# Optimization experiments

Measured on AMD Instinct MI355X. Metric: run time of the kernel, lower is better.

## Reference

```python
import jax, jax.numpy as jnp
import numpy as np

B, S, D = 4, 4096, 1024          # batch, seq, in/out features
H = 128                          # controller_hidden_dim
K = 8                            # num_spectral_bases
R = 8                            # low_rank_rank
OR = 8                           # orthogonal_rank
RES_SCALE = 1.0; SPEC_SCALE = 1.0; LR_SCALE = 1.0; ROT_SCALE = 1.0
LN_EPS = 1e-5


def setup_inputs() -> dict:
    key = jax.random.key(0)
    ks = jax.random.split(key, 16)
    g = lambda k, shape, scale=0.02: jax.random.normal(k, shape, jnp.float32) * scale
    return dict(
        x=jax.random.normal(ks[0], (B, S, D), jnp.float32),
        # base linear (teacher-aligned base)
        W_base=g(ks[1], (D, D)), b_base=jnp.zeros((D,), jnp.float32),
        # pooled-token conditioner: LayerNorm -> Linear -> GELU -> Linear
        ln_g=jnp.ones((D,), jnp.float32), ln_b=jnp.zeros((D,), jnp.float32),
        Wc1=g(ks[2], (D, H)), bc1=jnp.zeros((H,), jnp.float32),
        Wc2=g(ks[3], (H, H)), bc2=jnp.zeros((H,), jnp.float32),
        # gate heads
        W_rot_gate=g(ks[4], (H, 1)), b_rot_gate=jnp.zeros((1,), jnp.float32),
        W_rot_coeff=g(ks[5], (H, OR)), b_rot_coeff=jnp.zeros((OR,), jnp.float32),
        W_spec_gate=g(ks[6], (H, K)), b_spec_gate=jnp.zeros((K,), jnp.float32),
        W_lr_coeff=g(ks[7], (H, R)), b_lr_coeff=jnp.zeros((R,), jnp.float32),
        # spectral basis operator: input basis U, output basis V
        U_spec=g(ks[8], (K, D), 0.05), V_spec=g(ks[9], (K, D), 0.05),
        # low-rank residual operator
        U_lr=g(ks[10], (R, D), 0.05), V_lr=g(ks[11], (R, D), 0.05),
        # low-rank orthogonal mixer generators (skew-symmetric pairs)
        A_orth=g(ks[12], (OR, D), 0.05), B_orth=g(ks[13], (OR, D), 0.05),
    )


def reference(x, W_base, b_base, ln_g, ln_b, Wc1, bc1, Wc2, bc2,
              W_rot_gate, b_rot_gate, W_rot_coeff, b_rot_coeff,
              W_spec_gate, b_spec_gate, W_lr_coeff, b_lr_coeff,
              U_spec, V_spec, U_lr, V_lr, A_orth, B_orth):
    # --- pooled token conditioner: mean pool -> LN -> MLP -> hidden h [B,H]
    pooled = x.mean(axis=1)                                   # [B, D]
    mu = pooled.mean(-1, keepdims=True)
    var = pooled.var(-1, keepdims=True)
    z = (pooled - mu) * jax.lax.rsqrt(var + LN_EPS) * ln_g + ln_b
    h = jax.nn.gelu(z @ Wc1 + bc1) @ Wc2 + bc2                # [B, H]

    # --- conditioner-produced gates
    rot_gate = jax.nn.sigmoid(h @ W_rot_gate + b_rot_gate)    # [B, 1]
    rot_coeff = jnp.tanh(h @ W_rot_coeff + b_rot_coeff)       # [B, OR]
    spec_gate = jnp.tanh(h @ W_spec_gate + b_spec_gate)       # [B, K]
    lr_coeff = jnp.tanh(h @ W_lr_coeff + b_lr_coeff)          # [B, R]

    # --- low-rank orthogonal mixer: x_rot = x + gate * x @ G^T,
    #     G = sum_k c_k (a_k b_k^T - b_k a_k^T) (skew-symmetric generator)
    pa = jnp.einsum('bsi,ki->bsk', x, A_orth)
    pb = jnp.einsum('bsi,ki->bsk', x, B_orth)
    rot = (jnp.einsum('bsk,bk,ki->bsi', pb, rot_coeff, A_orth)
           - jnp.einsum('bsk,bk,ki->bsi', pa, rot_coeff, B_orth))
    x_rot = x + (ROT_SCALE * rot_gate)[:, None, :] * rot      # [B,S,D]

    # --- spectral basis operator: gated rank-K map through fixed bases
    s = jnp.einsum('bsi,ki->bsk', x_rot, U_spec)
    y_spec = SPEC_SCALE * jnp.einsum('bsk,bk,ko->bso', s, spec_gate, V_spec)

    # --- low-rank residual operator
    t = jnp.einsum('bsi,ki->bsk', x_rot, U_lr)
    y_lr = LR_SCALE * jnp.einsum('bsk,bk,ko->bso', t, lr_coeff, V_lr)

    # --- teacher-aligned base + gated residual operators
    return x_rot @ W_base + b_base + RES_SCALE * (y_spec + y_lr)
```

## Files before the change

kernel.cpp:

```cpp
#include <hip/hip_runtime.h>

typedef unsigned short u16;
typedef unsigned int   u32;
typedef __bf16 bf16x8 __attribute__((ext_vector_type(8)));
typedef float  f32x4  __attribute__((ext_vector_type(4)));

#define DD 1024

__device__ __forceinline__ u16 f2bf(float f) {
  u32 u = __float_as_uint(f);
  u32 r = (u + 0x7FFFu + ((u >> 16) & 1u)) >> 16;
  return (u16)r;
}

typedef const __attribute__((address_space(1))) void* gp1;
typedef __attribute__((address_space(3))) void* lp3;
__device__ __forceinline__ void gll16(const void* g, void* l) {
  __builtin_amdgcn_global_load_lds((gp1)g, (lp3)l, 16, 0, 0);
}

template <bool XB>
__global__ __launch_bounds__(256) void k01_pre(
    const float* __restrict__ x, u16* __restrict__ xb, float* __restrict__ pooled,
    const float* __restrict__ W,
    const float* __restrict__ Ao, const float* __restrict__ Bo,
    const float* __restrict__ Us, const float* __restrict__ Ul,
    float* __restrict__ AWBW, float* __restrict__ Mbuf,
    u16* __restrict__ Pb, u16* __restrict__ Wt) {
  const int tid = threadIdx.x;
  const int bid = blockIdx.x;
  if (bid >= 296) {
    const int i = bid - 296;
    const int xcd = i & 7, local = i >> 3;
    const int rb = xcd * 128 + local;
    const int b = rb >> 8;
    const long r0 = (long)rb * 16;
    const int c0 = tid * 4;
    float s0 = 0.f, s1 = 0.f, s2 = 0.f, s3 = 0.f;
    for (int r = 0; r < 16; r++) {
      float4 v = *(const float4*)(x + (r0 + r) * DD + c0);
      if (XB) {
        ushort4 o;
        o.x = f2bf(v.x); o.y = f2bf(v.y); o.z = f2bf(v.z); o.w = f2bf(v.w);
        *(ushort4*)(xb + (r0 + r) * DD + c0) = o;
      }
      s0 += v.x; s1 += v.y; s2 += v.z; s3 += v.w;
    }
    atomicAdd(&pooled[b * DD + c0 + 0], s0);
    atomicAdd(&pooled[b * DD + c0 + 1], s1);
    atomicAdd(&pooled[b * DD + c0 + 2], s2);
    atomicAdd(&pooled[b * DD + c0 + 3], s3);
    return;
  }
  if (bid < 32) {
    __shared__ float red2[2][128][16];
    const int m = bid;
    const int n = (m & 7) * 128 + (tid & 127), q = m >> 3, ih = tid >> 7;
    float acc[16];
#pragma unroll
    for (int k = 0; k < 16; k++) acc[k] = 0.f;
    const int ib = q * 256 + ih * 128;
    for (int i = ib; i < ib + 128; i++) {
      float wv = W[(long)i * DD + n];
#pragma unroll
      for (int k = 0; k < 8; k++) {
        acc[k]     += Ao[k * DD + i] * wv;
        acc[k + 8] += Bo[k * DD + i] * wv;
      }
    }
#pragma unroll
    for (int k = 0; k < 16; k++) red2[ih][tid & 127][k] = acc[k];
    __syncthreads();
    if (ih == 0)
#pragma unroll
      for (int k = 0; k < 16; k++)
        atomicAdd(&AWBW[k * DD + n], red2[0][tid][k] + red2[1][tid][k]);
  } else if (bid < 36) {
    __shared__ float red[64][4];
    const int m = bid - 32;
    const float* L  = (m == 0 || m == 2) ? Ao : Bo;
    const float* Rr = (m < 2) ? Us : Ul;
    const int o = tid >> 2, ch = tid & 3;
    const int k = o >> 3, kp = o & 7;
    float a = 0.f;
    for (int i = ch * 256; i < ch * 256 + 256; i++)
      a += L[(long)k * DD + i] * Rr[(long)kp * DD + i];
    red[o][ch] = a;
    __syncthreads();
    if (tid < 64) Mbuf[m * 64 + tid] = red[tid][0] + red[tid][1] + red[tid][2] + red[tid][3];
  } else if (bid < 40) {
    const int m = bid - 36;
    const float* src = m == 0 ? Ao : m == 1 ? Bo : m == 2 ? Us : Ul;
#pragma unroll
    for (int j = 0; j < 8; j++)
      for (int q = 0; q < 4; q++) {
        int i = q * 256 + tid;
        Pb[(m * 8 + j) * DD + i] = f2bf(src[j * DD + i]);
      }
  } else {
    __shared__ u16 T[64][66];
    const int t = bid - 40, tr = t >> 4, tc = t & 15;
#pragma unroll
    for (int q2 = 0; q2 < 16; q2++) {
      int idx = q2 * 256 + tid, r = idx >> 6, c = idx & 63;
      T[r][c] = f2bf(W[(long)(tr * 64 + r) * DD + tc * 64 + c]);
    }
    __syncthreads();
#pragma unroll
    for (int q2 = 0; q2 < 16; q2++) {
      int idx = q2 * 256 + tid, c = idx >> 6, r = idx & 63;
      Wt[(long)(tc * 64 + c) * DD + tr * 64 + r] = T[r][c];
    }
  }
}

__global__ __launch_bounds__(256) void k2ab(
    const float* __restrict__ pooledsum,
    const float* __restrict__ lng, const float* __restrict__ lnb,
    const float* __restrict__ Wc1, float* __restrict__ h1pre,
    const float* __restrict__ AWBW, const float* Vs, const float* Vl,
    const float* bc1, const float* Wc2, const float* bc2,
    const float* Wrg, const float* brg, const float* Wrc, const float* brc,
    const float* Wsg, const float* bsg, const float* Wlc, const float* blc,
    float* __restrict__ gates, u16* __restrict__ RwT,
    u32* __restrict__ cnt) {
  const int tid = threadIdx.x;
  if (blockIdx.x < 32) {
    __shared__ float zs[1024];
    __shared__ float red[256];
    const int b = blockIdx.x >> 3, ch = blockIdx.x & 7;
    float4 v = *(const float4*)(pooledsum + b * DD + tid * 4);
    v.x *= (1.f / 4096.f); v.y *= (1.f / 4096.f); v.z *= (1.f / 4096.f); v.w *= (1.f / 4096.f);
    float s = v.x + v.y + v.z + v.w;
    float sq = v.x * v.x + v.y * v.y + v.z * v.z + v.w * v.w;
    red[tid] = s; __syncthreads();
    for (int st = 128; st > 0; st >>= 1) { if (tid < st) red[tid] += red[tid + st]; __syncthreads(); }
    float mu = red[0] * (1.f / 1024.f);
    __syncthreads();
    red[tid] = sq; __syncthreads();
    for (int st = 128; st > 0; st >>= 1) { if (tid < st) red[tid] += red[tid + st]; __syncthreads(); }
    float var = red[0] * (1.f / 1024.f) - mu * mu;
    float rs = rsqrtf(var + 1e-5f);
    __syncthreads();
    {
      float4 g = *(const float4*)(lng + tid * 4);
      float4 be = *(const float4*)(lnb + tid * 4);
      zs[tid * 4 + 0] = (v.x - mu) * rs * g.x + be.x;
      zs[tid * 4 + 1] = (v.y - mu) * rs * g.y + be.y;
      zs[tid * 4 + 2] = (v.z - mu) * rs * g.z + be.z;
      zs[tid * 4 + 3] = (v.w - mu) * rs * g.w + be.w;
    }
    __syncthreads();
    const int j = tid & 127, half = tid >> 7;
    float a = 0.f;
#pragma unroll 8
    for (int dd = 0; dd < 64; dd++) {
      int ldi = half * 64 + dd;
      a += zs[ch * 128 + ldi] * Wc1[(long)ch * 16384 + ldi * 128 + j];
    }
    red[tid] = a;
    __syncthreads();
    if (tid < 128) atomicAdd(&h1pre[b * 128 + tid], red[tid] + red[tid + 128]);
    __syncthreads();
    if (tid == 0) atomicAdd(cnt, 1u);
  } else if (blockIdx.x < 36) {
    __shared__ float h1s[128], hb[128];
    __shared__ float red[256];
    const int b = (int)blockIdx.x - 32;
    if (tid == 0) {
      while (atomicAdd(cnt, 0u) < 32u) __builtin_amdgcn_s_sleep(8);
    }
    __syncthreads();
    if (tid < 128) {
      float hv = atomicAdd(&h1pre[b * 128 + tid], 0.f) + bc1[tid];
      float th = tanhf(0.7978845608028654f * (hv + 0.044715f * hv * hv * hv));
      h1s[tid] = 0.5f * hv * (1.f + th);
    }
    __syncthreads();
    const int i = tid & 127, half = tid >> 7;
    float a = 0.f;
#pragma unroll 8
    for (int k = 0; k < 64; k++) {
      int kk = half * 64 + k;
      a += h1s[kk] * Wc2[kk * 128 + i];
    }
    red[tid] = a;
    __syncthreads();
    if (tid < 128) hb[tid] = red[tid] + red[tid + 128] + bc2[tid];
    __syncthreads();
    if (tid < 25) {
      float acc;
      if (tid == 0) {
        acc = brg[0];
        for (int k = 0; k < 128; k++) acc += hb[k] * Wrg[k];
        red[0] = 1.f / (1.f + expf(-acc));
      } else if (tid < 9) {
        int ci = tid - 1; acc = brc[ci];
        for (int k = 0; k < 128; k++) acc += hb[k] * Wrc[k * 8 + ci];
        red[tid] = tanhf(acc);
      } else if (tid < 17) {
        int ci = tid - 9; acc = bsg[ci];
        for (int k = 0; k < 128; k++) acc += hb[k] * Wsg[k * 8 + ci];
        red[tid] = tanhf(acc);
      } else {
        int ci = tid - 17; acc = blc[ci];
        for (int k = 0; k < 128; k++) acc += hb[k] * Wlc[k * 8 + ci];
        red[tid] = tanhf(acc);
      }
    }
    __syncthreads();
    if (tid < 24) {
      float g = red[0];
      gates[b * 32 + tid] = (tid < 8) ? g * red[1 + tid] : red[1 + tid];
    }
  } else {
    const int n = (int)(blockIdx.x - 36) * 256 + tid;
#pragma unroll
    for (int j = 0; j < 8; j++) {
      RwT[n * 32 + j]      = f2bf(AWBW[j * DD + n]);
      RwT[n * 32 + 8 + j]  = f2bf(AWBW[(8 + j) * DD + n]);
      RwT[n * 32 + 16 + j] = f2bf(Vs[(long)j * DD + n]);
      RwT[n * 32 + 24 + j] = f2bf(Vl[(long)j * DD + n]);
    }
  }
}

__global__ __launch_bounds__(256, 2) void k3b_fused(
    const u16* __restrict__ xb, const u16* __restrict__ Wt,
    const u16* __restrict__ Pb, const float* __restrict__ gates,
    const float* __restrict__ Mbuf, const u16* __restrict__ RwT,
    const float* __restrict__ bb, float* __restrict__ out) {
  __shared__ __align__(16) char smem[54400];
  const int tid = threadIdx.x, lane = tid & 63, w = tid >> 6;
  const int quad = lane >> 4, lrow = lane & 15;
  const int g = blockIdx.x;
  const int xcd = g & 7, local = g >> 3;
  const int bm = xcd * 16 + (local >> 2);
  const int bn2 = local & 3;
  const long m0 = (long)bm * 128;
  const int n0 = bn2 * 256;
  const int batch = bm >> 5;
  float* Ml = (float*)(smem + 53248);
  float* gl = (float*)(smem + 54272);
  Ml[tid] = Mbuf[tid];
  if (tid < 24) gl[tid] = gates[batch * 32 + tid];
  const int mw = (w & 1) * 64, nw = (w >> 1) * 128;
  const int pc0 = (w >> 1) * 16;
  const int sr = lane >> 2, sc = (lane & 3) * 16;
  const char* xbp = (const char*)xb;
  const char* wtp = (const char*)Wt;
  const char* pbp = (const char*)Pb;
  const long aOff0 = (m0 + (long)w * 16 + sr) * 2048 + sc;
  const long aOff1 = aOff0 + 64 * 2048;
  const long bOff  = ((long)n0 + w * 16 + sr) * 2048 + sc;
  const long pOff  = ((long)w * 16 + sr) * 2048 + sc;
  const int d0 = w * 1024 + lane * 16;

  f32x4 acc[4][8] = {};
  f32x4 acc2[4] = {};

  gll16(xbp + aOff0, smem + d0);
  gll16(xbp + aOff1, smem + d0 + 4096);
#pragma unroll
  for (int seg = 0; seg < 4; seg++)
    gll16(wtp + bOff + (long)seg * 64 * 2048, smem + 16384 + seg * 4096 + d0);
  if (w < 2) gll16(pbp + pOff, smem + 49152 + d0);
  __syncthreads();

  int cur = 0;
  for (int kc = 0; kc < 32; kc++) {
    if (kc < 31) {
      const long ko = (long)(kc + 1) * 64;
      const int s = cur ^ 1;
      gll16(xbp + aOff0 + ko, smem + s * 8192 + d0);
      gll16(xbp + aOff1 + ko, smem + s * 8192 + d0 + 4096);
#pragma unroll
      for (int seg = 0; seg < 4; seg++)
        gll16(wtp + bOff + (long)seg * 64 * 2048 + ko,
              smem + 16384 + s * 16384 + seg * 4096 + d0);
      if (w < 2) gll16(pbp + pOff + ko, smem + 49152 + s * 2048 + d0);
    }
    const u16* At = (const u16*)(smem + cur * 8192);
    const u16* Bt = (const u16*)(smem + 16384 + cur * 16384);
    const u16* Pt = (const u16*)(smem + 49152 + cur * 2048);
    bf16x8 af[4], bq[8], bp;
#pragma unroll
    for (int tm = 0; tm < 4; tm++)
      af[tm] = *(const bf16x8*)(At + (mw + tm * 16 + lrow) * 32 + quad * 8);
#pragma unroll
    for (int tn = 0; tn < 8; tn++)
      bq[tn] = *(const bf16x8*)(Bt + (nw + tn * 16 + lrow) * 32 + quad * 8);
    bp = *(const bf16x8*)(Pt + (pc0 + lrow) * 32 + quad * 8);
#pragma unroll
    for (int tm = 0; tm < 4; tm++)
#pragma unroll
      for (int tn = 0; tn < 8; tn++)
        acc[tm][tn] = __builtin_amdgcn_mfma_f32_16x16x32_bf16(af[tm], bq[tn], acc[tm][tn], 0, 0, 0);
#pragma unroll
    for (int tm = 0; tm < 4; tm++)
      acc2[tm] = __builtin_amdgcn_mfma_f32_16x16x32_bf16(af[tm], bp, acc2[tm], 0, 0, 0);
    __syncthreads();
    cur ^= 1;
  }

  {
    const long rOff = ((long)n0 + w * 16 + sr) * 64 + sc;
#pragma unroll
    for (int seg = 0; seg < 4; seg++)
      gll16((const char*)RwT + rOff + (long)seg * 64 * 64,
            smem + 16384 + seg * 4096 + d0);
  }
  float* projF = (float*)smem;
#pragma unroll
  for (int tm = 0; tm < 4; tm++)
#pragma unroll
    for (int r = 0; r < 4; r++) {
      int row = mw + tm * 16 + quad * 4 + r;
      int col = pc0 + lrow;
      projF[row * 32 + (col ^ (row & 31))] = acc2[tm][r];
    }
  __syncthreads();
  if (tid < 128) {
    float pr[32];
#pragma unroll
    for (int j = 0; j < 32; j++) pr[j] = projF[tid * 32 + (j ^ (tid & 31))];
    float wo[32];
#pragma unroll
    for (int k = 0; k < 8; k++) { wo[k] = gl[k] * pr[8 + k]; wo[8 + k] = -gl[k] * pr[k]; }
#pragma unroll
    for (int kp = 0; kp < 8; kp++) {
      float sv = pr[16 + kp], tv = pr[24 + kp];
#pragma unroll
      for (int k = 0; k < 8; k++) {
        float gpb = gl[k] * pr[8 + k], gpa = gl[k] * pr[k];
        sv += gpb * Ml[k * 8 + kp]       - gpa * Ml[64 + k * 8 + kp];
        tv += gpb * Ml[128 + k * 8 + kp] - gpa * Ml[192 + k * 8 + kp];
      }
      wo[16 + kp] = gl[8 + kp] * sv;
      wo[24 + kp] = gl[16 + kp] * tv;
    }
    u16* wLds = (u16*)(smem + 32768);
#pragma unroll
    for (int j = 0; j < 32; j++) wLds[tid * 32 + j] = f2bf(wo[j]);
  }
  __syncthreads();
  {
    const u16* wL = (const u16*)(smem + 32768);
    const u16* Rt = (const u16*)(smem + 16384);
    bf16x8 af[4], bq[8];
#pragma unroll
    for (int tm = 0; tm < 4; tm++)
      af[tm] = *(const bf16x8*)(wL + (mw + tm * 16 + lrow) * 32 + quad * 8);
#pragma unroll
    for (int tn = 0; tn < 8; tn++)
      bq[tn] = *(const bf16x8*)(Rt + (nw + tn * 16 + lrow) * 32 + quad * 8);
#pragma unroll
    for (int tm = 0; tm < 4; tm++)
#pragma unroll
      for (int tn = 0; tn < 8; tn++)
        acc[tm][tn] = __builtin_amdgcn_mfma_f32_16x16x32_bf16(af[tm], bq[tn], acc[tm][tn], 0, 0, 0);
  }
#pragma unroll
  for (int tn = 0; tn < 8; tn++) {
    const int col = n0 + nw + tn * 16 + lrow;
    const float bias = bb[col];
#pragma unroll
    for (int tm = 0; tm < 4; tm++)
#pragma unroll
      for (int r = 0; r < 4; r++) {
        long row = m0 + mw + tm * 16 + quad * 4 + r;
        out[row * DD + col] = acc[tm][tn][r] + bias;
      }
  }
}

template <bool XB>
__global__ __launch_bounds__(256) void k3_fused(
    const float* __restrict__ xf, const u16* __restrict__ xb,
    const u16* __restrict__ Wt, const u16* __restrict__ Pb,
    const float* __restrict__ gates, const float* __restrict__ Mbuf,
    const u16* __restrict__ RwT, const float* __restrict__ bb,
    float* __restrict__ out) {
  __shared__ __align__(16) u16 At[4096];
  __shared__ __align__(16) u16 Bt[4096];
  __shared__ __align__(16) u16 Pt[1024];
  __shared__ float projF[128 * 32];
  __shared__ __align__(16) u16 wLds[4096];
  __shared__ float Ml[256];
  __shared__ float gl[24];
  const int tid = threadIdx.x, lane = tid & 63, w = tid >> 6;
  const int quad = lane >> 4, lrow = lane & 15;
  const int bn = blockIdx.x & 7, bm = blockIdx.x >> 3;
  const long m0 = (long)bm * 128;
  const int n0 = bn * 128;
  const int batch = bm >> 5;
  Ml[tid] = Mbuf[tid];
  if (tid < 24) gl[tid] = gates[batch * 32 + tid];
  const int mw = (w & 1) * 64, nw = (w >> 1) * 64;
  const int p0 = (w * 2) * 1024 + lane * 16, p1 = p0 + 1024;
  f32x4 acc[4][4] = {};
  f32x4 acc2[2][2] = {};
  for (int kc = 0; kc < 32; kc++) {
    uint4 vb0 = *(const uint4*)((const char*)Wt + (long)(n0 + (p0 >> 6)) * 2048 + kc * 64 + (p0 & 63));
    uint4 vb1 = *(const uint4*)((const char*)Wt + (long)(n0 + (p1 >> 6)) * 2048 + kc * 64 + (p1 & 63));
    uint4 vp;
    if (tid < 128)
      vp = *(const uint4*)((const char*)Pb + (tid >> 2) * 2048 + kc * 64 + (tid & 3) * 16);
    if (XB) {
      uint4 va0 = *(const uint4*)((const char*)xb + (m0 + (p0 >> 6)) * 2048 + kc * 64 + (p0 & 63));
      uint4 va1 = *(const uint4*)((const char*)xb + (m0 + (p1 >> 6)) * 2048 + kc * 64 + (p1 & 63));
      *(uint4*)((char*)At + p0) = va0;
      *(uint4*)((char*)At + p1) = va1;
    } else {
      ushort4 oa[4];
#pragma unroll
      for (int i = 0; i < 4; i++) {
        int fi = i * 256 + tid, row = fi >> 3, c4 = (fi & 7) * 4;
        float4 v = *(const float4*)(xf + (m0 + row) * DD + kc * 32 + c4);
        oa[i].x = f2bf(v.x); oa[i].y = f2bf(v.y); oa[i].z = f2bf(v.z); oa[i].w = f2bf(v.w);
      }
#pragma unroll
      for (int i = 0; i < 4; i++) {
        int fi = i * 256 + tid, row = fi >> 3, c4 = (fi & 7) * 4;
        *(ushort4*)(At + row * 32 + c4) = oa[i];
      }
    }
    *(uint4*)((char*)Bt + p0) = vb0;
    *(uint4*)((char*)Bt + p1) = vb1;
    if (tid < 128) *(uint4*)((char*)Pt + (tid >> 2) * 64 + (tid & 3) * 16) = vp;
    __syncthreads();
    bf16x8 af[4], bq[4], af2[2], bp[2];
#pragma unroll
    for (int tm = 0; tm < 4; tm++)
      af[tm] = *(const bf16x8*)(At + (mw + tm * 16 + lrow) * 32 + quad * 8);
#pragma unroll
    for (int tn = 0; tn < 4; tn++)
      bq[tn] = *(const bf16x8*)(Bt + (nw + tn * 16 + lrow) * 32 + quad * 8);
#pragma unroll
    for (int t2 = 0; t2 < 2; t2++)
      af2[t2] = *(const bf16x8*)(At + (w * 32 + t2 * 16 + lrow) * 32 + quad * 8);
#pragma unroll
    for (int tn2 = 0; tn2 < 2; tn2++)
      bp[tn2] = *(const bf16x8*)(Pt + (tn2 * 16 + lrow) * 32 + quad * 8);
#pragma unroll
    for (int tm = 0; tm < 4; tm++)
#pragma unroll
      for (int tn = 0; tn < 4; tn++)
        acc[tm][tn] = __builtin_amdgcn_mfma_f32_16x16x32_bf16(af[tm], bq[tn], acc[tm][tn], 0, 0, 0);
#pragma unroll
    for (int t2 = 0; t2 < 2; t2++)
#pragma unroll
      for (int tn2 = 0; tn2 < 2; tn2++)
        acc2[t2][tn2] = __builtin_amdgcn_mfma_f32_16x16x32_bf16(af2[t2], bp[tn2], acc2[t2][tn2], 0, 0, 0);
    __syncthreads();
  }
#pragma unroll
  for (int t2 = 0; t2 < 2; t2++)
#pragma unroll
    for (int tn2 = 0; tn2 < 2; tn2++)
#pragma unroll
      for (int r = 0; r < 4; r++)
        projF[(w * 32 + t2 * 16 + quad * 4 + r) * 32 + tn2 * 16 + lrow] = acc2[t2][tn2][r];
  {
    uint4 vr0 = *(const uint4*)((const char*)RwT + (long)(n0 + (p0 >> 6)) * 64 + (p0 & 63));
    uint4 vr1 = *(const uint4*)((const char*)RwT + (long)(n0 + (p1 >> 6)) * 64 + (p1 & 63));
    *(uint4*)((char*)Bt + p0) = vr0;
    *(uint4*)((char*)Bt + p1) = vr1;
  }
  __syncthreads();
  if (tid < 128) {
    float pr[32];
#pragma unroll
    for (int j = 0; j < 32; j++) pr[j] = projF[tid * 32 + j];
    float wo[32];
#pragma unroll
    for (int k = 0; k < 8; k++) { wo[k] = gl[k] * pr[8 + k]; wo[8 + k] = -gl[k] * pr[k]; }
#pragma unroll
    for (int kp = 0; kp < 8; kp++) {
      float sv = pr[16 + kp], tv = pr[24 + kp];
#pragma unroll
      for (int k = 0; k < 8; k++) {
        float gpb = gl[k] * pr[8 + k], gpa = gl[k] * pr[k];
        sv += gpb * Ml[k * 8 + kp]       - gpa * Ml[64 + k * 8 + kp];
        tv += gpb * Ml[128 + k * 8 + kp] - gpa * Ml[192 + k * 8 + kp];
      }
      wo[16 + kp] = gl[8 + kp] * sv;
      wo[24 + kp] = gl[16 + kp] * tv;
    }
#pragma unroll
    for (int j = 0; j < 32; j++) wLds[tid * 32 + j] = f2bf(wo[j]);
  }
  __syncthreads();
  {
    bf16x8 af[4], bq[4];
#pragma unroll
    for (int tm = 0; tm < 4; tm++)
      af[tm] = *(const bf16x8*)(wLds + (mw + tm * 16 + lrow) * 32 + quad * 8);
#pragma unroll
    for (int tn = 0; tn < 4; tn++)
      bq[tn] = *(const bf16x8*)(Bt + (nw + tn * 16 + lrow) * 32 + quad * 8);
#pragma unroll
    for (int tm = 0; tm < 4; tm++)
#pragma unroll
      for (int tn = 0; tn < 4; tn++)
        acc[tm][tn] = __builtin_amdgcn_mfma_f32_16x16x32_bf16(af[tm], bq[tn], acc[tm][tn], 0, 0, 0);
  }
#pragma unroll
  for (int tn = 0; tn < 4; tn++) {
    const int col = n0 + nw + tn * 16 + lrow;
    const float bias = bb[col];
#pragma unroll
    for (int tm = 0; tm < 4; tm++)
#pragma unroll
      for (int r = 0; r < 4; r++) {
        long row = m0 + mw + tm * 16 + quad * 4 + r;
        out[row * DD + col] = acc[tm][tn][r] + bias;
      }
  }
}

extern "C" void kernel_launch(void* const* d_in, const int* in_sizes, int n_in,
                              void* d_out, int out_size, void* d_ws, size_t ws_size,
                              hipStream_t stream) {
  const float* x   = (const float*)d_in[0];
  const float* Wb  = (const float*)d_in[1];
  const float* bb  = (const float*)d_in[2];
  const float* lng = (const float*)d_in[3];
  const float* lnb = (const float*)d_in[4];
  const float* Wc1 = (const float*)d_in[5];
  const float* bc1 = (const float*)d_in[6];
  const float* Wc2 = (const float*)d_in[7];
  const float* bc2 = (const float*)d_in[8];
  const float* Wrg = (const float*)d_in[9];
  const float* brg = (const float*)d_in[10];
  const float* Wrc = (const float*)d_in[11];
  const float* brc = (const float*)d_in[12];
  const float* Wsg = (const float*)d_in[13];
  const float* bsg = (const float*)d_in[14];
  const float* Wlc = (const float*)d_in[15];
  const float* blc = (const float*)d_in[16];
  const float* Us  = (const float*)d_in[17];
  const float* Vs  = (const float*)d_in[18];
  const float* Ul  = (const float*)d_in[19];
  const float* Vl  = (const float*)d_in[20];
  const float* Ao  = (const float*)d_in[21];
  const float* Bo  = (const float*)d_in[22];

  char* ws = (char*)d_ws;
  float* pooled = (float*)(ws + 0);
  float* AWBW   = (float*)(ws + 16384);
  float* h1pre  = (float*)(ws + 81920);
  float* gates  = (float*)(ws + 83968);
  float* Mbuf   = (float*)(ws + 84480);
  u32*   cntH   = (u32*)  (ws + 85504);
  u16*   RwT    = (u16*)  (ws + 85568);
  u16*   Pb     = (u16*)  (ws + 151104);
  u16*   Wt     = (u16*)  (ws + 216640);
  u16*   xb     = (u16*)  (ws + 2313792);
  float* out    = (float*)d_out;

  const bool modeA = ws_size >= (size_t)2313792 + 33554432;

  (void)hipMemsetAsync(d_ws, 0, 85568, stream);
  if (modeA) {
    k01_pre<true><<<1320, 256, 0, stream>>>(x, xb, pooled, Wb, Ao, Bo, Us, Ul,
                                            AWBW, Mbuf, Pb, Wt);
    k2ab<<<40, 256, 0, stream>>>(pooled, lng, lnb, Wc1, h1pre,
                                 AWBW, Vs, Vl, bc1, Wc2, bc2,
                                 Wrg, brg, Wrc, brc, Wsg, bsg, Wlc, blc,
                                 gates, RwT, cntH);
    k3b_fused<<<512, 256, 0, stream>>>(xb, Wt, Pb, gates, Mbuf, RwT, bb, out);
  } else {
    k01_pre<false><<<1320, 256, 0, stream>>>(x, xb, pooled, Wb, Ao, Bo, Us, Ul,
                                             AWBW, Mbuf, Pb, Wt);
    k2ab<<<40, 256, 0, stream>>>(pooled, lng, lnb, Wc1, h1pre,
                                 AWBW, Vs, Vl, bc1, Wc2, bc2,
                                 Wrg, brg, Wrc, brc, Wsg, bsg, Wlc, blc,
                                 gates, RwT, cntH);
    k3_fused<false><<<1024, 256, 0, stream>>>(x, xb, Wt, Pb, gates, Mbuf, RwT, bb, out);
  }
}
```

Before: 311.4 us.

## Split preprocessing into weight-prep and x-streaming kernels, widen AW/BW projection grid

The fused preprocessing kernel is split into two launches: one for weight-derived work (AW/BW projection, small Gram products, bf16 packing, W transpose) and one that streams x to bf16 and accumulates the pooled sums. The AW/BW projection now uses 64 blocks, each covering half as many input rows, which shortens the long-running blocks that previously held up the combined grid. Static shared arrays are merged into one aliased buffer so fewer LDS bytes are reserved per block. The cost is an extra kernel launch and the loss of overlap between the two kinds of work within a single grid.

```diff
diff --git a/kernel.cpp b/kernel.cpp
--- a/kernel.cpp
+++ b/kernel.cpp
@@ -19,48 +19,24 @@
   __builtin_amdgcn_global_load_lds((gp1)g, (lp3)l, 16, 0, 0);
 }
 
-template <bool XB>
-__global__ __launch_bounds__(256) void k01_pre(
-    const float* __restrict__ x, u16* __restrict__ xb, float* __restrict__ pooled,
+__global__ __launch_bounds__(256) void kA_heavy(
     const float* __restrict__ W,
     const float* __restrict__ Ao, const float* __restrict__ Bo,
     const float* __restrict__ Us, const float* __restrict__ Ul,
     float* __restrict__ AWBW, float* __restrict__ Mbuf,
     u16* __restrict__ Pb, u16* __restrict__ Wt) {
+  __shared__ __align__(16) char shb[16384];
   const int tid = threadIdx.x;
   const int bid = blockIdx.x;
-  if (bid >= 296) {
-    const int i = bid - 296;
-    const int xcd = i & 7, local = i >> 3;
-    const int rb = xcd * 128 + local;
-    const int b = rb >> 8;
-    const long r0 = (long)rb * 16;
-    const int c0 = tid * 4;
-    float s0 = 0.f, s1 = 0.f, s2 = 0.f, s3 = 0.f;
-    for (int r = 0; r < 16; r++) {
-      float4 v = *(const float4*)(x + (r0 + r) * DD + c0);
-      if (XB) {
-        ushort4 o;
-        o.x = f2bf(v.x); o.y = f2bf(v.y); o.z = f2bf(v.z); o.w = f2bf(v.w);
-        *(ushort4*)(xb + (r0 + r) * DD + c0) = o;
-      }
-      s0 += v.x; s1 += v.y; s2 += v.z; s3 += v.w;
-    }
-    atomicAdd(&pooled[b * DD + c0 + 0], s0);
-    atomicAdd(&pooled[b * DD + c0 + 1], s1);
-    atomicAdd(&pooled[b * DD + c0 + 2], s2);
-    atomicAdd(&pooled[b * DD + c0 + 3], s3);
-    return;
-  }
-  if (bid < 32) {
-    __shared__ float red2[2][128][16];
+  if (bid < 64) {
+    float (*red2)[128][16] = (float (*)[128][16])shb;
     const int m = bid;
     const int n = (m & 7) * 128 + (tid & 127), q = m >> 3, ih = tid >> 7;
     float acc[16];
 #pragma unroll
     for (int k = 0; k < 16; k++) acc[k] = 0.f;
-    const int ib = q * 256 + ih * 128;
-    for (int i = ib; i < ib + 128; i++) {
+    const int ib = q * 128 + ih * 64;
+    for (int i = ib; i < ib + 64; i++) {
       float wv = W[(long)i * DD + n];
 #pragma unroll
       for (int k = 0; k < 8; k++) {
@@ -75,9 +51,9 @@
 #pragma unroll
       for (int k = 0; k < 16; k++)
         atomicAdd(&AWBW[k * DD + n], red2[0][tid][k] + red2[1][tid][k]);
-  } else if (bid < 36) {
-    __shared__ float red[64][4];
-    const int m = bid - 32;
+  } else if (bid < 68) {
+    float (*red)[4] = (float (*)[4])shb;
+    const int m = bid - 64;
     const float* L  = (m == 0 || m == 2) ? Ao : Bo;
     const float* Rr = (m < 2) ? Us : Ul;
     const int o = tid >> 2, ch = tid & 3;
@@ -88,8 +64,8 @@
     red[o][ch] = a;
     __syncthreads();
     if (tid < 64) Mbuf[m * 64 + tid] = red[tid][0] + red[tid][1] + red[tid][2] + red[tid][3];
-  } else if (bid < 40) {
-    const int m = bid - 36;
+  } else if (bid < 72) {
+    const int m = bid - 68;
     const float* src = m == 0 ? Ao : m == 1 ? Bo : m == 2 ? Us : Ul;
 #pragma unroll
     for (int j = 0; j < 8; j++)
@@ -98,8 +74,8 @@
         Pb[(m * 8 + j) * DD + i] = f2bf(src[j * DD + i]);
       }
   } else {
-    __shared__ u16 T[64][66];
-    const int t = bid - 40, tr = t >> 4, tc = t & 15;
+    u16 (*T)[66] = (u16 (*)[66])shb;
+    const int t = bid - 72, tr = t >> 4, tc = t & 15;
 #pragma unroll
     for (int q2 = 0; q2 < 16; q2++) {
       int idx = q2 * 256 + tid, r = idx >> 6, c = idx & 63;
@@ -112,6 +88,32 @@
       Wt[(long)(tc * 64 + c) * DD + tr * 64 + r] = T[r][c];
     }
   }
+}
+
+template <bool XB>
+__global__ __launch_bounds__(256) void kB_stream(
+    const float* __restrict__ x, u16* __restrict__ xb,
+    float* __restrict__ pooled) {
+  const int i = blockIdx.x;
+  const int xcd = i & 7, local = i >> 3;
+  const int rb = xcd * 128 + local;
+  const int b = rb >> 8;
+  const long r0 = (long)rb * 16;
+  const int c0 = threadIdx.x * 4;
+  float s0 = 0.f, s1 = 0.f, s2 = 0.f, s3 = 0.f;
+  for (int r = 0; r < 16; r++) {
+    float4 v = *(const float4*)(x + (r0 + r) * DD + c0);
+    if (XB) {
+      ushort4 o;
+      o.x = f2bf(v.x); o.y = f2bf(v.y); o.z = f2bf(v.z); o.w = f2bf(v.w);
+      *(ushort4*)(xb + (r0 + r) * DD + c0) = o;
+    }
+    s0 += v.x; s1 += v.y; s2 += v.z; s3 += v.w;
+  }
+  atomicAdd(&pooled[b * DD + c0 + 0], s0);
+  atomicAdd(&pooled[b * DD + c0 + 1], s1);
+  atomicAdd(&pooled[b * DD + c0 + 2], s2);
+  atomicAdd(&pooled[b * DD + c0 + 3], s3);
 }
 
 __global__ __launch_bounds__(256) void k2ab(
@@ -562,21 +564,17 @@
   const bool modeA = ws_size >= (size_t)2313792 + 33554432;
 
   (void)hipMemsetAsync(d_ws, 0, 85568, stream);
-  if (modeA) {
-    k01_pre<true><<<1320, 256, 0, stream>>>(x, xb, pooled, Wb, Ao, Bo, Us, Ul,
-                                            AWBW, Mbuf, Pb, Wt);
-    k2ab<<<40, 256, 0, stream>>>(pooled, lng, lnb, Wc1, h1pre,
-                                 AWBW, Vs, Vl, bc1, Wc2, bc2,
-                                 Wrg, brg, Wrc, brc, Wsg, bsg, Wlc, blc,
-                                 gates, RwT, cntH);
+  kA_heavy<<<328, 256, 0, stream>>>(Wb, Ao, Bo, Us, Ul, AWBW, Mbuf, Pb, Wt);
+  if (modeA)
+    kB_stream<true><<<1024, 256, 0, stream>>>(x, xb, pooled);
+  else
+    kB_stream<false><<<1024, 256, 0, stream>>>(x, xb, pooled);
+  k2ab<<<40, 256, 0, stream>>>(pooled, lng, lnb, Wc1, h1pre,
+                               AWBW, Vs, Vl, bc1, Wc2, bc2,
+                               Wrg, brg, Wrc, brc, Wsg, bsg, Wlc, blc,
+                               gates, RwT, cntH);
+  if (modeA)
     k3b_fused<<<512, 256, 0, stream>>>(xb, Wt, Pb, gates, Mbuf, RwT, bb, out);
-  } else {
-    k01_pre<false><<<1320, 256, 0, stream>>>(x, xb, pooled, Wb, Ao, Bo, Us, Ul,
-                                             AWBW, Mbuf, Pb, Wt);
-    k2ab<<<40, 256, 0, stream>>>(pooled, lng, lnb, Wc1, h1pre,
-                                 AWBW, Vs, Vl, bc1, Wc2, bc2,
-                                 Wrg, brg, Wrc, brc, Wsg, bsg, Wlc, blc,
-                                 gates, RwT, cntH);
+  else
     k3_fused<false><<<1024, 256, 0, stream>>>(x, xb, Wt, Pb, gates, Mbuf, RwT, bb, out);
-  }
-}
+}
```

Result: faster. 290.1 us (-6.8%).
